# Kernel optimization log

Hardware: AMD Instinct MI355X
Metric: run time of the kernel (lower is better)

## Reference

```python
import jax, jax.numpy as jnp
from jax import lax
import numpy as np

NUM_TAGS = 128
B, S = 256, 512


def setup_inputs() -> dict:
    key = jax.random.key(0)
    k1, k2, k3 = jax.random.split(key, 3)
    emissions = jax.random.normal(k1, (B, S, NUM_TAGS), dtype=jnp.float32)
    tags = jax.random.randint(k2, (B, S), 0, NUM_TAGS, dtype=jnp.int64)
    mask = jnp.ones((B, S), dtype=bool)
    transitions = jax.random.normal(k3, (NUM_TAGS, NUM_TAGS), dtype=jnp.float32)
    return {"emissions": emissions, "tags": tags, "mask": mask, "transitions": transitions}


def reference(emissions, tags, mask, transitions):
    # emissions: [B,S,C], tags: [B,S] int, mask: [B,S] bool, transitions: [C,C]
    m = mask.astype(emissions.dtype)

    # --- gold score (vectorized over time) ---
    emit = jnp.take_along_axis(emissions, tags[..., None], axis=2)[..., 0]  # [B,S]
    trans = transitions[tags[:, :-1], tags[:, 1:]]                           # [B,S-1]
    gold = jnp.sum(emit * m) + jnp.sum(trans * m[:, 1:])

    # --- partition via forward algorithm (note: original masks cancel out:
    # alpha*mask + alpha*~mask == alpha, so partition ignores mask) ---
    def step(alpha, e_t):
        # alpha: [B,C] prev log-alpha, e_t: [B,C] emissions at t
        score = alpha[:, :, None] + transitions[None, :, :] + e_t[:, None, :]  # [B,C,C]
        return jax.nn.logsumexp(score, axis=1), None

    alpha0 = emissions[:, 0]                       # [B,C]
    em_rest = jnp.swapaxes(emissions[:, 1:], 0, 1) # [S-1,B,C]
    alpha, _ = lax.scan(step, alpha0, em_rest)
    partition = jnp.sum(jax.nn.logsumexp(alpha, axis=1))

    # forward returns -log_likelihood = partition - gold
    return partition - gold
```

## Files before the change

### kernel.cpp

```cpp
#include <hip/hip_runtime.h>

#define NT 128
#define SS 512
#define PW 132

typedef float f32x2 __attribute__((ext_vector_type(2)));

__device__ __forceinline__ float rdlane(float v, int lane) {
    return __int_as_float(__builtin_amdgcn_readlane(__float_as_int(v), lane));
}
__device__ __forceinline__ int fexp_of(float x) {
    return (int)((__float_as_uint(x) >> 23) & 0xFFu) - 127;
}
__device__ __forceinline__ void lds_barrier() {
    asm volatile("s_waitcnt lgkmcnt(0)\n\ts_barrier" ::: "memory");
}

__global__ void zero_out_kernel(float* out) { out[0] = 0.0f; }

__global__ __launch_bounds__(256, 1) void crf_fwd_kernel(
    const float* __restrict__ emissions,
    const int* __restrict__ tags,
    const unsigned char* __restrict__ mask,
    const float* __restrict__ trans,
    float* __restrict__ out)
{
    const int b   = blockIdx.x;
    const int tid = threadIdx.x;
    const int l   = tid & 63;
    const int w   = tid >> 6;
    const int st  = (w << 5) + (l & 31);

    __shared__ float pbuf[2][4 * PW];
    __shared__ int   kbuf[4];
    __shared__ float redf[4];
    __shared__ float redg[4];

    const float*         emB = emissions + (size_t)b * SS * NT;
    const int*           tgB = tags + b * SS;
    const unsigned char* mkB = mask + b * SS;

    float gold = 0.0f;
    for (int t = tid; t < SS; t += 256) {
        int tg   = tgB[t];
        float mk = mkB[t] ? 1.0f : 0.0f;
        float a  = emB[(size_t)t * NT + tg];
        if (t > 0) a += trans[tgB[t - 1] * NT + tg];
        gold += a * mk;
    }

    f32x2 eTr[32];
    #pragma unroll
    for (int r = 0; r < 32; r++) {
        const float* row = trans + (size_t)((w << 5) + r) * NT;
        f32x2 v; v.x = __expf(row[l]); v.y = __expf(row[l + 64]);
        eTr[r] = v;
    }

    float a0 = emB[st];
    {
        float v = a0;
        #pragma unroll
        for (int o = 16; o > 0; o >>= 1) v = fmaxf(v, __shfl_xor(v, o));
        if (l == 0) redf[w] = v;
    }
    __syncthreads();
    const float M0 = fmaxf(fmaxf(redf[0], redf[1]), fmaxf(redf[2], redf[3]));

    float p = __expf(a0 - M0);
    float S = 0.0f;
    int K = 0, kv_own = 0;

    float ex_o = __expf(emB[(size_t)1 * NT + st]);
    float ex_e = __expf(emB[(size_t)2 * NT + st]);
    float pd_o = emB[(size_t)3 * NT + st];
    float pd_e = emB[(size_t)4 * NT + st];

    auto matvec = [&](int q, bool kw) -> float {
        f32x2 A0 = {0.f,0.f}, A1 = {0.f,0.f}, A2 = {0.f,0.f}, A3 = {0.f,0.f};
        #pragma unroll
        for (int r = 0; r < 32; r += 4) {
            float q0 = rdlane(p, r + 0);
            float q1 = rdlane(p, r + 1);
            float q2 = rdlane(p, r + 2);
            float q3 = rdlane(p, r + 3);
            f32x2 b0 = {q0, q0}, b1 = {q1, q1}, b2 = {q2, q2}, b3 = {q3, q3};
            A0 = __builtin_elementwise_fma(b0, eTr[r + 0], A0);
            A1 = __builtin_elementwise_fma(b1, eTr[r + 1], A1);
            A2 = __builtin_elementwise_fma(b2, eTr[r + 2], A2);
            A3 = __builtin_elementwise_fma(b3, eTr[r + 3], A3);
        }
        f32x2 s2 = (A0 + A1) + (A2 + A3);
        pbuf[q][w * PW + l]      = s2.x;
        pbuf[q][w * PW + l + 64] = s2.y;
        if (kw && l == 0) kbuf[w] = kv_own;
        lds_barrier();
        return (pbuf[q][0 * PW + st] + pbuf[q][1 * PW + st]) +
               (pbuf[q][2 * PW + st] + pbuf[q][3 * PW + st]);
    };
    auto rot = [&](int t, float& pd, float& ex) {
        float nr = pd;
        int tn = t + 4; if (tn > SS - 1) tn = SS - 1;
        pd = emB[(size_t)tn * NT + st];
        ex = __expf(nr);
    };

    #pragma unroll 1
    for (int t = 1; t < SS; t += 4) {
        {
            float sn = matvec(1, false) * ex_o;
            p = ldexpf(sn, -K);
            S += (float)K;
            int kv = fexp_of(p);
            #pragma unroll
            for (int o = 16; o > 0; o >>= 1) kv = max(kv, __shfl_xor(kv, o));
            kv_own = kv;
            rot(t, pd_o, ex_o);
        }
        if (t + 1 < SS) {
            float sn = matvec(0, true) * ex_e;
            int k0 = kbuf[0], k1 = kbuf[1], k2 = kbuf[2], k3 = kbuf[3];
            K = max(max(k0, k1), max(k2, k3));
            p = sn;
            rot(t + 1, pd_e, ex_e);
        }
        if (t + 2 < SS) { p = matvec(1, false) * ex_o; rot(t + 2, pd_o, ex_o); }
        if (t + 3 < SS) { p = matvec(0, false) * ex_e; rot(t + 3, pd_e, ex_e); }
    }

    {
        float sw = (l < 32) ? p : 0.0f;
        float g  = gold;
        #pragma unroll
        for (int o = 32; o > 0; o >>= 1) {
            sw += __shfl_xor(sw, o);
            g  += __shfl_xor(g, o);
        }
        if (l == 0) { redf[w] = sw; redg[w] = g; }
    }
    __syncthreads();
    if (tid == 0) {
        float tot  = (redf[0] + redf[1]) + (redf[2] + redf[3]);
        float part = M0 + S * 0.69314718055994531f + __logf(tot);
        float gt   = (redg[0] + redg[1]) + (redg[2] + redg[3]);
        atomicAdd(out, part - gt);
    }
}

extern "C" void kernel_launch(void* const* d_in, const int* in_sizes, int n_in,
                              void* d_out, int out_size, void* d_ws, size_t ws_size,
                              hipStream_t stream) {
    const float*         emissions = (const float*)d_in[0];
    const int*           tags      = (const int*)d_in[1];
    const unsigned char* mask      = (const unsigned char*)d_in[2];
    const float*         trans     = (const float*)d_in[3];
    float*               out       = (float*)d_out;

    zero_out_kernel<<<1, 1, 0, stream>>>(out);
    crf_fwd_kernel<<<256, 256, 0, stream>>>(emissions, tags, mask, trans, out);
}
```

Baseline: 240.2 us.

## Split CRF forward matvec across eight wavefronts instead of four

Doubles the block to 512 threads so each of eight waves owns 16 source tags instead of 32, halving the per-step readlane/FMA chain in the serial forward recursion. The price is an eight-way LDS partial-sum reduction per step and a barrier across twice as many waves. The gold-score loop becomes a single pass per thread because SS equals the block size.

```diff
diff --git a/kernel.cpp b/kernel.cpp
--- a/kernel.cpp
+++ b/kernel.cpp
@@ -3,6 +3,7 @@
 #define NT 128
 #define SS 512
 #define PW 132
+#define NW 8
 
 typedef float f32x2 __attribute__((ext_vector_type(2)));
 
@@ -18,7 +19,7 @@
 
 __global__ void zero_out_kernel(float* out) { out[0] = 0.0f; }
 
-__global__ __launch_bounds__(256, 1) void crf_fwd_kernel(
+__global__ __launch_bounds__(512, 1) void crf_fwd_kernel(
     const float* __restrict__ emissions,
     const int* __restrict__ tags,
     const unsigned char* __restrict__ mask,
@@ -29,30 +30,31 @@
     const int tid = threadIdx.x;
     const int l   = tid & 63;
     const int w   = tid >> 6;
-    const int st  = (w << 5) + (l & 31);
+    const int st  = (w << 4) + (l & 15);
 
-    __shared__ float pbuf[2][4 * PW];
-    __shared__ int   kbuf[4];
-    __shared__ float redf[4];
-    __shared__ float redg[4];
+    __shared__ float pbuf[2][NW * PW];
+    __shared__ int   kbuf[NW];
+    __shared__ float redf[NW];
+    __shared__ float redg[NW];
 
     const float*         emB = emissions + (size_t)b * SS * NT;
     const int*           tgB = tags + b * SS;
     const unsigned char* mkB = mask + b * SS;
 
     float gold = 0.0f;
-    for (int t = tid; t < SS; t += 256) {
+    {
+        int t    = tid;
         int tg   = tgB[t];
         float mk = mkB[t] ? 1.0f : 0.0f;
         float a  = emB[(size_t)t * NT + tg];
         if (t > 0) a += trans[tgB[t - 1] * NT + tg];
-        gold += a * mk;
+        gold = a * mk;
     }
 
-    f32x2 eTr[32];
+    f32x2 eTr[16];
     #pragma unroll
-    for (int r = 0; r < 32; r++) {
-        const float* row = trans + (size_t)((w << 5) + r) * NT;
+    for (int r = 0; r < 16; r++) {
+        const float* row = trans + (size_t)((w << 4) + r) * NT;
         f32x2 v; v.x = __expf(row[l]); v.y = __expf(row[l + 64]);
         eTr[r] = v;
     }
@@ -61,11 +63,16 @@
     {
         float v = a0;
         #pragma unroll
-        for (int o = 16; o > 0; o >>= 1) v = fmaxf(v, __shfl_xor(v, o));
+        for (int o = 8; o > 0; o >>= 1) v = fmaxf(v, __shfl_xor(v, o));
         if (l == 0) redf[w] = v;
     }
     __syncthreads();
-    const float M0 = fmaxf(fmaxf(redf[0], redf[1]), fmaxf(redf[2], redf[3]));
+    float M0;
+    {
+        float m01 = fmaxf(redf[0], redf[1]), m23 = fmaxf(redf[2], redf[3]);
+        float m45 = fmaxf(redf[4], redf[5]), m67 = fmaxf(redf[6], redf[7]);
+        M0 = fmaxf(fmaxf(m01, m23), fmaxf(m45, m67));
+    }
 
     float p = __expf(a0 - M0);
     float S = 0.0f;
@@ -79,7 +86,7 @@
     auto matvec = [&](int q, bool kw) -> float {
         f32x2 A0 = {0.f,0.f}, A1 = {0.f,0.f}, A2 = {0.f,0.f}, A3 = {0.f,0.f};
         #pragma unroll
-        for (int r = 0; r < 32; r += 4) {
+        for (int r = 0; r < 16; r += 4) {
             float q0 = rdlane(p, r + 0);
             float q1 = rdlane(p, r + 1);
             float q2 = rdlane(p, r + 2);
@@ -95,8 +102,11 @@
         pbuf[q][w * PW + l + 64] = s2.y;
         if (kw && l == 0) kbuf[w] = kv_own;
         lds_barrier();
-        return (pbuf[q][0 * PW + st] + pbuf[q][1 * PW + st]) +
-               (pbuf[q][2 * PW + st] + pbuf[q][3 * PW + st]);
+        float r0 = pbuf[q][0 * PW + st], r1 = pbuf[q][1 * PW + st];
+        float r2 = pbuf[q][2 * PW + st], r3 = pbuf[q][3 * PW + st];
+        float r4 = pbuf[q][4 * PW + st], r5 = pbuf[q][5 * PW + st];
+        float r6 = pbuf[q][6 * PW + st], r7 = pbuf[q][7 * PW + st];
+        return ((r0 + r1) + (r2 + r3)) + ((r4 + r5) + (r6 + r7));
     };
     auto rot = [&](int t, float& pd, float& ex) {
         float nr = pd;
@@ -113,13 +123,14 @@
             S += (float)K;
             int kv = fexp_of(p);
             #pragma unroll
-            for (int o = 16; o > 0; o >>= 1) kv = max(kv, __shfl_xor(kv, o));
+            for (int o = 8; o > 0; o >>= 1) kv = max(kv, __shfl_xor(kv, o));
             kv_own = kv;
             rot(t, pd_o, ex_o);
         }
         if (t + 1 < SS) {
             float sn = matvec(0, true) * ex_e;
-            int k0 = kbuf[0], k1 = kbuf[1], k2 = kbuf[2], k3 = kbuf[3];
+            int k0 = max(kbuf[0], kbuf[1]), k1 = max(kbuf[2], kbuf[3]);
+            int k2 = max(kbuf[4], kbuf[5]), k3 = max(kbuf[6], kbuf[7]);
             K = max(max(k0, k1), max(k2, k3));
             p = sn;
             rot(t + 1, pd_e, ex_e);
@@ -129,7 +140,7 @@
     }
 
     {
-        float sw = (l < 32) ? p : 0.0f;
+        float sw = (l < 16) ? p : 0.0f;
         float g  = gold;
         #pragma unroll
         for (int o = 32; o > 0; o >>= 1) {
@@ -140,9 +151,11 @@
     }
     __syncthreads();
     if (tid == 0) {
-        float tot  = (redf[0] + redf[1]) + (redf[2] + redf[3]);
+        float tot = ((redf[0] + redf[1]) + (redf[2] + redf[3])) +
+                    ((redf[4] + redf[5]) + (redf[6] + redf[7]));
+        float gt  = ((redg[0] + redg[1]) + (redg[2] + redg[3])) +
+                    ((redg[4] + redg[5]) + (redg[6] + redg[7]));
         float part = M0 + S * 0.69314718055994531f + __logf(tot);
-        float gt   = (redg[0] + redg[1]) + (redg[2] + redg[3]);
         atomicAdd(out, part - gt);
     }
 }
@@ -157,5 +170,5 @@
     float*               out       = (float*)d_out;
 
     zero_out_kernel<<<1, 1, 0, stream>>>(out);
-    crf_fwd_kernel<<<256, 256, 0, stream>>>(emissions, tags, mask, trans, out);
+    crf_fwd_kernel<<<256, 512, 0, stream>>>(emissions, tags, mask, trans, out);
 }
```

Result: slower. 254.8 us (+6.1%).
